# Optimization experiments

Measured on AMD Instinct MI355X. Metric: run time of the kernel, lower is better.

The kernel has to match this reference:

```python
import jax, jax.numpy as jnp
import numpy as np

B, S, I, H, O = 32, 64, 256, 256, 128


def setup_inputs() -> dict:
    key = jax.random.key(0)
    ks = jax.random.split(key, 8)
    init_k = 1.0 / np.sqrt(H)
    F = H + I
    return {
        "sentence": jax.random.normal(ks[0], (B, S, I), dtype=jnp.float32),
        "weight": jax.random.uniform(ks[1], (H, F), minval=-init_k, maxval=init_k, dtype=jnp.float32),
        "weight_lambda": jax.random.uniform(ks[2], (H, F), minval=0.0, maxval=1.0, dtype=jnp.float32),
        "weight_gamma": jax.random.uniform(ks[3], (H, F), minval=-0.001 * init_k, maxval=0.001 * init_k, dtype=jnp.float32),
        "bias": jax.random.uniform(ks[4], (H,), minval=-init_k, maxval=init_k, dtype=jnp.float32),
        "out_w": jax.random.uniform(ks[5], (O, H), minval=-init_k, maxval=init_k, dtype=jnp.float32),
        "out_b": jax.random.uniform(ks[6], (O,), minval=-init_k, maxval=init_k, dtype=jnp.float32),
    }


def reference(sentence, weight, weight_lambda, weight_gamma, bias, out_w, out_b):
    b, s, i = sentence.shape
    h_dim = weight.shape[0]
    f_dim = weight.shape[1]  # h_dim + i
    h0 = jnp.zeros((b, h_dim), dtype=sentence.dtype)
    f0 = jnp.zeros((b, h_dim, f_dim), dtype=sentence.dtype)

    def step(carry, x_t):
        h, f = carry
        total_input = jnp.concatenate([x_t, h], axis=1)          # (b, f_dim)
        total_weights = weight + f                                # (b, h, f_dim)
        pre = jnp.einsum('bf,bhf->bh', total_input, total_weights)
        norm = jnp.sqrt(jnp.sum(total_weights * total_weights, axis=2)) + 1e-16  # (b, h)
        h_new = jnp.tanh(pre / norm + bias)
        f_new = weight_lambda * (f / norm[..., None]) + \
                weight_gamma * jnp.einsum('bh,bf->bhf', h_new, total_input)
        return (h_new, f_new), None

    (h_fin, f_fin), _ = jax.lax.scan(step, (h0, f0), jnp.swapaxes(sentence, 0, 1))
    tag_space = h_fin @ out_w.T + out_b
    return tag_space, h_fin, f_fin
```

## Files before the change

### kernel.cpp

```cpp
#include <hip/hip_runtime.h>

#define Bq 32
#define Sq 64
#define Iq 256
#define Hq 256
#define Oq 128
#define Fq 512
#define WPB 8
#define NT 512
#define PRE_S 56

__global__ __launch_bounds__(NT, 2) void stpn_main(
    const float* __restrict__ x,
    const float* __restrict__ w,
    const float* __restrict__ wl,
    const float* __restrict__ wgm,
    const float* __restrict__ bias,
    const float* __restrict__ ow,
    const float* __restrict__ ob,
    float* __restrict__ out,
    unsigned long long* __restrict__ hb)
{
    const int blk   = blockIdx.x;
    const int b     = blk & 31;
    const int chunk = blk >> 5;
    const int h0    = chunk * 32;
    const int tid   = threadIdx.x;
    const int lr    = tid & 15;
    const int r     = tid >> 4;
    const int row   = h0 + r;

    __shared__ float ti[2][Fq];
    __shared__ float xall[PRE_S * Iq];

    float fw[32], fl[32], fg[32], ff[32];
    const size_t rowoff = (size_t)row * Fq;
#pragma unroll
    for (int j = 0; j < 8; ++j) {
        const int c = 4 * lr + 64 * j;
        *(float4*)&fw[4*j] = *(const float4*)(w   + rowoff + c);
        *(float4*)&fl[4*j] = *(const float4*)(wl  + rowoff + c);
        *(float4*)&fg[4*j] = *(const float4*)(wgm + rowoff + c);
    }
#pragma unroll
    for (int j = 0; j < 32; ++j) ff[j] = 0.f;

    {
        const float4* xs = (const float4*)(x + (size_t)b * Sq * Iq);
        float4* xd = (float4*)xall;
#pragma unroll
        for (int k = 0; k < (PRE_S * Iq / 4) / NT; ++k)
            xd[tid + NT * k] = xs[tid + NT * k];
    }
    const float brow = bias[row];
    const float* xb = x + (size_t)b * Sq * Iq;

    for (int t = 0; t < Sq; ++t) {
        const int p = t & 1;
        if (tid < Iq) {
            if (t >= PRE_S) ti[p][tid] = xb[(size_t)t * Iq + tid];
        } else {
            const int hh = tid - Iq;
            float hv = 0.f;
            if (t > 0) {
                unsigned long long* slot =
                    hb + (size_t)((t - 1) & 1) * Bq * Hq + (size_t)b * Hq + hh;
                unsigned long long v;
                do {
                    v = __hip_atomic_load(slot, __ATOMIC_RELAXED,
                                          __HIP_MEMORY_SCOPE_AGENT);
                } while ((unsigned)(v >> 32) != (unsigned)t);
                hv = __uint_as_float((unsigned)(v & 0xffffffffu));
            }
            ti[p][Iq + hh] = hv;
        }
        __syncthreads();

        const float* xpart = (t < PRE_S) ? (xall + t * Iq) : &ti[p][0];
        const float* hpart = &ti[p][Iq];

        float pre = 0.f, nsq = 0.f;
#pragma unroll
        for (int j = 0; j < 4; ++j) {
            const float4 tv = *(const float4*)&xpart[4 * lr + 64 * j];
            float tw;
            tw = fw[4*j+0] + ff[4*j+0]; pre = fmaf(tv.x, tw, pre); nsq = fmaf(tw, tw, nsq);
            tw = fw[4*j+1] + ff[4*j+1]; pre = fmaf(tv.y, tw, pre); nsq = fmaf(tw, tw, nsq);
            tw = fw[4*j+2] + ff[4*j+2]; pre = fmaf(tv.z, tw, pre); nsq = fmaf(tw, tw, nsq);
            tw = fw[4*j+3] + ff[4*j+3]; pre = fmaf(tv.w, tw, pre); nsq = fmaf(tw, tw, nsq);
        }
#pragma unroll
        for (int j = 4; j < 8; ++j) {
            const float4 tv = *(const float4*)&hpart[4 * lr + 64 * (j - 4)];
            float tw;
            tw = fw[4*j+0] + ff[4*j+0]; pre = fmaf(tv.x, tw, pre); nsq = fmaf(tw, tw, nsq);
            tw = fw[4*j+1] + ff[4*j+1]; pre = fmaf(tv.y, tw, pre); nsq = fmaf(tw, tw, nsq);
            tw = fw[4*j+2] + ff[4*j+2]; pre = fmaf(tv.z, tw, pre); nsq = fmaf(tw, tw, nsq);
            tw = fw[4*j+3] + ff[4*j+3]; pre = fmaf(tv.w, tw, pre); nsq = fmaf(tw, tw, nsq);
        }
#pragma unroll
        for (int m = 1; m < 16; m <<= 1) {
            pre += __shfl_xor(pre, m, 16);
            nsq += __shfl_xor(nsq, m, 16);
        }
        const float inv = __fdividef(1.0f, sqrtf(nsq) + 1e-16f);
        const float hn  = tanhf(fmaf(pre, inv, brow));

        if (lr == 0) {
            const unsigned long long pk =
                ((unsigned long long)(unsigned)(t + 1) << 32) |
                (unsigned long long)__float_as_uint(hn);
            __hip_atomic_store(
                hb + (size_t)p * Bq * Hq + (size_t)b * Hq + row, pk,
                __ATOMIC_RELAXED, __HIP_MEMORY_SCOPE_AGENT);
        }

#pragma unroll
        for (int j = 0; j < 4; ++j) {
            const float4 tv = *(const float4*)&xpart[4 * lr + 64 * j];
            ff[4*j+0] = fmaf(fl[4*j+0], ff[4*j+0] * inv, fg[4*j+0] * (hn * tv.x));
            ff[4*j+1] = fmaf(fl[4*j+1], ff[4*j+1] * inv, fg[4*j+1] * (hn * tv.y));
            ff[4*j+2] = fmaf(fl[4*j+2], ff[4*j+2] * inv, fg[4*j+2] * (hn * tv.z));
            ff[4*j+3] = fmaf(fl[4*j+3], ff[4*j+3] * inv, fg[4*j+3] * (hn * tv.w));
        }
#pragma unroll
        for (int j = 4; j < 8; ++j) {
            const float4 tv = *(const float4*)&hpart[4 * lr + 64 * (j - 4)];
            ff[4*j+0] = fmaf(fl[4*j+0], ff[4*j+0] * inv, fg[4*j+0] * (hn * tv.x));
            ff[4*j+1] = fmaf(fl[4*j+1], ff[4*j+1] * inv, fg[4*j+1] * (hn * tv.y));
            ff[4*j+2] = fmaf(fl[4*j+2], ff[4*j+2] * inv, fg[4*j+2] * (hn * tv.z));
            ff[4*j+3] = fmaf(fl[4*j+3], ff[4*j+3] * inv, fg[4*j+3] * (hn * tv.w));
        }
    }

    float* fo = out + Bq * Oq + Bq * Hq + (size_t)b * Hq * Fq + rowoff;
#pragma unroll
    for (int j = 0; j < 8; ++j) {
        const int c = 4 * lr + 64 * j;
        *(float4*)(fo + c) = *(const float4*)&ff[4*j];
    }

    if (chunk == 0) {
        if (tid < Hq) {
            unsigned long long* slot =
                hb + (size_t)1 * Bq * Hq + (size_t)b * Hq + tid;
            unsigned long long v;
            do {
                v = __hip_atomic_load(slot, __ATOMIC_RELAXED,
                                      __HIP_MEMORY_SCOPE_AGENT);
            } while ((unsigned)(v >> 32) != (unsigned)Sq);
            const float hv = __uint_as_float((unsigned)(v & 0xffffffffu));
            ti[0][tid] = hv;
            out[Bq * Oq + (size_t)b * Hq + tid] = hv;
        }
        __syncthreads();
        const int o = tid >> 2;
        const int l = tid & 3;
        const float* wr = ow + (size_t)o * Hq;
        float acc = 0.f;
#pragma unroll
        for (int k = 0; k < 16; ++k) {
            const int cc = 16 * k + 4 * l;
            const float4 w4 = *(const float4*)(wr + cc);
            const float4 h4 = *(const float4*)&ti[0][cc];
            acc += w4.x * h4.x + w4.y * h4.y + w4.z * h4.z + w4.w * h4.w;
        }
        acc += __shfl_xor(acc, 1, 4);
        acc += __shfl_xor(acc, 2, 4);
        if (l == 0) out[(size_t)b * Oq + o] = acc + ob[o];
    }
}

extern "C" void kernel_launch(void* const* d_in, const int* in_sizes, int n_in,
                              void* d_out, int out_size, void* d_ws, size_t ws_size,
                              hipStream_t stream)
{
    const float* x    = (const float*)d_in[0];
    const float* w    = (const float*)d_in[1];
    const float* wl   = (const float*)d_in[2];
    const float* wgm  = (const float*)d_in[3];
    const float* bias = (const float*)d_in[4];
    const float* ow   = (const float*)d_in[5];
    const float* ob   = (const float*)d_in[6];
    float* out = (float*)d_out;

    hipMemsetAsync(d_ws, 0, 2 * Bq * Hq * sizeof(unsigned long long), stream);

    stpn_main<<<Bq * WPB, NT, 0, stream>>>(x, w, wl, wgm, bias, ow, ob, out,
                                           (unsigned long long*)d_ws);
}
```

Baseline: 164.1 us.

## Replace per-step block barrier with per-wavefront polling and shuffle broadcast of h

Each wavefront now polls all 256 hidden-state slots itself, 4 per lane, and spreads them to lanes with shuffles. This removes the shared-memory staging and the __syncthreads that every timestep needed. The whole input sequence (64 steps) is also preloaded into LDS, so the late-step global loads of x go away. The cost is redundant global polling traffic from every wave and a larger LDS footprint (64KB per block), which may limit occupancy.

```diff
diff --git a/kernel.cpp b/kernel.cpp
--- a/kernel.cpp
+++ b/kernel.cpp
@@ -8,7 +8,6 @@
 #define Fq 512
 #define WPB 8
 #define NT 512
-#define PRE_S 56
 
 __global__ __launch_bounds__(NT, 2) void stpn_main(
     const float* __restrict__ x,
@@ -29,9 +28,9 @@
     const int lr    = tid & 15;
     const int r     = tid >> 4;
     const int row   = h0 + r;
+    const int ln    = tid & 63;
 
-    __shared__ float ti[2][Fq];
-    __shared__ float xall[PRE_S * Iq];
+    __shared__ float xall[Sq * Iq];
 
     float fw[32], fl[32], fg[32], ff[32];
     const size_t rowoff = (size_t)row * Fq;
@@ -49,35 +48,42 @@
         const float4* xs = (const float4*)(x + (size_t)b * Sq * Iq);
         float4* xd = (float4*)xall;
 #pragma unroll
-        for (int k = 0; k < (PRE_S * Iq / 4) / NT; ++k)
+        for (int k = 0; k < (Sq * Iq / 4) / NT; ++k)
             xd[tid + NT * k] = xs[tid + NT * k];
     }
     const float brow = bias[row];
-    const float* xb = x + (size_t)b * Sq * Iq;
+    __syncthreads();
 
     for (int t = 0; t < Sq; ++t) {
-        const int p = t & 1;
-        if (tid < Iq) {
-            if (t >= PRE_S) ti[p][tid] = xb[(size_t)t * Iq + tid];
-        } else {
-            const int hh = tid - Iq;
-            float hv = 0.f;
-            if (t > 0) {
-                unsigned long long* slot =
-                    hb + (size_t)((t - 1) & 1) * Bq * Hq + (size_t)b * Hq + hh;
-                unsigned long long v;
-                do {
-                    v = __hip_atomic_load(slot, __ATOMIC_RELAXED,
-                                          __HIP_MEMORY_SCOPE_AGENT);
-                } while ((unsigned)(v >> 32) != (unsigned)t);
-                hv = __uint_as_float((unsigned)(v & 0xffffffffu));
-            }
-            ti[p][Iq + hh] = hv;
+        float hv0 = 0.f, hv1 = 0.f, hv2 = 0.f, hv3 = 0.f;
+        if (t > 0) {
+            const unsigned tt = (unsigned)t;
+            unsigned long long* s0 =
+                hb + (size_t)((t - 1) & 1) * Bq * Hq + (size_t)b * Hq + ln;
+            unsigned long long v0, v1, v2, v3;
+            do {
+                v0 = __hip_atomic_load(s0,       __ATOMIC_RELAXED, __HIP_MEMORY_SCOPE_AGENT);
+                v1 = __hip_atomic_load(s0 + 64,  __ATOMIC_RELAXED, __HIP_MEMORY_SCOPE_AGENT);
+                v2 = __hip_atomic_load(s0 + 128, __ATOMIC_RELAXED, __HIP_MEMORY_SCOPE_AGENT);
+                v3 = __hip_atomic_load(s0 + 192, __ATOMIC_RELAXED, __HIP_MEMORY_SCOPE_AGENT);
+            } while (!((unsigned)(v0 >> 32) == tt && (unsigned)(v1 >> 32) == tt &&
+                       (unsigned)(v2 >> 32) == tt && (unsigned)(v3 >> 32) == tt));
+            hv0 = __uint_as_float((unsigned)(v0 & 0xffffffffu));
+            hv1 = __uint_as_float((unsigned)(v1 & 0xffffffffu));
+            hv2 = __uint_as_float((unsigned)(v2 & 0xffffffffu));
+            hv3 = __uint_as_float((unsigned)(v3 & 0xffffffffu));
         }
-        __syncthreads();
+        float hp[4][4];
+        const int src = 4 * lr;
+#pragma unroll
+        for (int e = 0; e < 4; ++e) {
+            hp[0][e] = __shfl(hv0, src + e, 64);
+            hp[1][e] = __shfl(hv1, src + e, 64);
+            hp[2][e] = __shfl(hv2, src + e, 64);
+            hp[3][e] = __shfl(hv3, src + e, 64);
+        }
 
-        const float* xpart = (t < PRE_S) ? (xall + t * Iq) : &ti[p][0];
-        const float* hpart = &ti[p][Iq];
+        const float* xpart = xall + t * Iq;
 
         float pre = 0.f, nsq = 0.f;
 #pragma unroll
@@ -91,12 +97,12 @@
         }
 #pragma unroll
         for (int j = 4; j < 8; ++j) {
-            const float4 tv = *(const float4*)&hpart[4 * lr + 64 * (j - 4)];
+            const int jj = j - 4;
             float tw;
-            tw = fw[4*j+0] + ff[4*j+0]; pre = fmaf(tv.x, tw, pre); nsq = fmaf(tw, tw, nsq);
-            tw = fw[4*j+1] + ff[4*j+1]; pre = fmaf(tv.y, tw, pre); nsq = fmaf(tw, tw, nsq);
-            tw = fw[4*j+2] + ff[4*j+2]; pre = fmaf(tv.z, tw, pre); nsq = fmaf(tw, tw, nsq);
-            tw = fw[4*j+3] + ff[4*j+3]; pre = fmaf(tv.w, tw, pre); nsq = fmaf(tw, tw, nsq);
+            tw = fw[4*j+0] + ff[4*j+0]; pre = fmaf(hp[jj][0], tw, pre); nsq = fmaf(tw, tw, nsq);
+            tw = fw[4*j+1] + ff[4*j+1]; pre = fmaf(hp[jj][1], tw, pre); nsq = fmaf(tw, tw, nsq);
+            tw = fw[4*j+2] + ff[4*j+2]; pre = fmaf(hp[jj][2], tw, pre); nsq = fmaf(tw, tw, nsq);
+            tw = fw[4*j+3] + ff[4*j+3]; pre = fmaf(hp[jj][3], tw, pre); nsq = fmaf(tw, tw, nsq);
         }
 #pragma unroll
         for (int m = 1; m < 16; m <<= 1) {
@@ -111,7 +117,7 @@
                 ((unsigned long long)(unsigned)(t + 1) << 32) |
                 (unsigned long long)__float_as_uint(hn);
             __hip_atomic_store(
-                hb + (size_t)p * Bq * Hq + (size_t)b * Hq + row, pk,
+                hb + (size_t)(t & 1) * Bq * Hq + (size_t)b * Hq + row, pk,
                 __ATOMIC_RELAXED, __HIP_MEMORY_SCOPE_AGENT);
         }
 
@@ -125,11 +131,11 @@
         }
 #pragma unroll
         for (int j = 4; j < 8; ++j) {
-            const float4 tv = *(const float4*)&hpart[4 * lr + 64 * (j - 4)];
-            ff[4*j+0] = fmaf(fl[4*j+0], ff[4*j+0] * inv, fg[4*j+0] * (hn * tv.x));
-            ff[4*j+1] = fmaf(fl[4*j+1], ff[4*j+1] * inv, fg[4*j+1] * (hn * tv.y));
-            ff[4*j+2] = fmaf(fl[4*j+2], ff[4*j+2] * inv, fg[4*j+2] * (hn * tv.z));
-            ff[4*j+3] = fmaf(fl[4*j+3], ff[4*j+3] * inv, fg[4*j+3] * (hn * tv.w));
+            const int jj = j - 4;
+            ff[4*j+0] = fmaf(fl[4*j+0], ff[4*j+0] * inv, fg[4*j+0] * (hn * hp[jj][0]));
+            ff[4*j+1] = fmaf(fl[4*j+1], ff[4*j+1] * inv, fg[4*j+1] * (hn * hp[jj][1]));
+            ff[4*j+2] = fmaf(fl[4*j+2], ff[4*j+2] * inv, fg[4*j+2] * (hn * hp[jj][2]));
+            ff[4*j+3] = fmaf(fl[4*j+3], ff[4*j+3] * inv, fg[4*j+3] * (hn * hp[jj][3]));
         }
     }
 
@@ -141,6 +147,7 @@
     }
 
     if (chunk == 0) {
+        float* hbuf = xall;
         if (tid < Hq) {
             unsigned long long* slot =
                 hb + (size_t)1 * Bq * Hq + (size_t)b * Hq + tid;
@@ -150,7 +157,7 @@
                                       __HIP_MEMORY_SCOPE_AGENT);
             } while ((unsigned)(v >> 32) != (unsigned)Sq);
             const float hv = __uint_as_float((unsigned)(v & 0xffffffffu));
-            ti[0][tid] = hv;
+            hbuf[tid] = hv;
             out[Bq * Oq + (size_t)b * Hq + tid] = hv;
         }
         __syncthreads();
@@ -162,7 +169,7 @@
         for (int k = 0; k < 16; ++k) {
             const int cc = 16 * k + 4 * l;
             const float4 w4 = *(const float4*)(wr + cc);
-            const float4 h4 = *(const float4*)&ti[0][cc];
+            const float4 h4 = *(const float4*)&hbuf[cc];
             acc += w4.x * h4.x + w4.y * h4.y + w4.z * h4.z + w4.w * h4.w;
         }
         acc += __shfl_xor(acc, 1, 4);
```

New measurement: 309.2 us. +88.5%, slower.
